# Kernel optimization log

Hardware: AMD Instinct MI355X
Metric: run time of the kernel (lower is better)

## Reference

```python
import jax, jax.numpy as jnp
import numpy as np

N_HEAD = 8
GROUPS = 16
EPS = 1e-5
C = 256


def group_norm(x, gamma, beta):
    # x: (B, C, H, W); GroupNorm over (C//G, H, W) within each group
    B, Cc, H, W = x.shape
    xg = x.reshape(B, GROUPS, Cc // GROUPS, H * W)
    mu = xg.mean(axis=(2, 3), keepdims=True)
    var = xg.var(axis=(2, 3), keepdims=True)
    xn = ((xg - mu) * jax.lax.rsqrt(var + EPS)).reshape(B, Cc, H, W)
    return xn * gamma[None, :, None, None] + beta[None, :, None, None]


def cross_attn(q, k, v, channel):
    # q, k, v: (B, n_head, head_dim, H, W); full bidirectional spatial attention
    B, n, d, H, W = q.shape
    scores = jnp.einsum('bnchw,bncyx->bnhwyx', q, k) / np.float32(np.sqrt(channel))
    attn = jax.nn.softmax(scores.reshape(B, n, H, W, H * W), axis=-1)
    attn = attn.reshape(B, n, H, W, H, W)
    out = jnp.einsum('bnhwyx,bncyx->bnchw', attn, v)
    return out.reshape(B, n * d, H, W)


def conv1x1(w, x, b=None):
    # w: (Cout, Cin), x: (B, Cin, H, W)
    y = jnp.einsum('oc,bchw->bohw', w, x)
    if b is not None:
        y = y + b[None, :, None, None]
    return y


def setup_inputs() -> dict:
    key = jax.random.key(0)
    ks = jax.random.split(key, 8)
    B, H, W = 16, 32, 32
    s = 1.0 / np.sqrt(C)
    return {
        'x_A': jax.random.normal(ks[0], (B, C, H, W), jnp.float32),
        'x_B': jax.random.normal(ks[1], (B, C, H, W), jnp.float32),
        'gA': jnp.ones((C,), jnp.float32),
        'bA': jnp.zeros((C,), jnp.float32),
        'gB': jnp.ones((C,), jnp.float32),
        'bB': jnp.zeros((C,), jnp.float32),
        'WqkvA': jax.random.normal(ks[2], (3 * C, C), jnp.float32) * s,
        'WqkvB': jax.random.normal(ks[3], (3 * C, C), jnp.float32) * s,
        'WoutA': jax.random.normal(ks[4], (C, C), jnp.float32) * s,
        'boutA': jnp.zeros((C,), jnp.float32),
        'WoutB': jax.random.normal(ks[5], (C, C), jnp.float32) * s,
        'boutB': jnp.zeros((C,), jnp.float32),
    }


def reference(x_A, x_B, gA, bA, gB, bB, WqkvA, WqkvB, WoutA, boutA, WoutB, boutB):
    B, Cc, H, W = x_A.shape
    d = Cc // N_HEAD
    norm_A = group_norm(x_A, gA, bA)
    norm_B = group_norm(x_B, gB, bB)
    qkvA = conv1x1(WqkvA, norm_A).reshape(B, N_HEAD, 3 * d, H, W)
    qA, kA, vA = jnp.split(qkvA, 3, axis=2)
    qkvB = conv1x1(WqkvB, norm_B).reshape(B, N_HEAD, 3 * d, H, W)
    qB, kB, vB = jnp.split(qkvB, 3, axis=2)
    # A branch attends query_B -> key/value_A (note scale uses full channel count)
    out_A = conv1x1(WoutA, cross_attn(qB, kA, vA, Cc), boutA) + norm_A
    out_B = conv1x1(WoutB, cross_attn(qA, kB, vB, Cc), boutB) + norm_B
    return (out_A, out_B)
```

## Files before the change

kernel.cpp:

```cpp
#include <hip/hip_runtime.h>
#include <hip/hip_bf16.h>
#include <math.h>

typedef __attribute__((ext_vector_type(8))) short short8;
typedef __attribute__((ext_vector_type(4))) short short4_;
typedef __attribute__((ext_vector_type(4))) float f32x4;
typedef __attribute__((ext_vector_type(4))) unsigned int uint4_;

#define MFMA16(a, b, c) __builtin_amdgcn_mfma_f32_16x16x32_bf16((a), (b), (c), 0, 0, 0)

__device__ __forceinline__ short f2bf(float f) {
  union { float f; unsigned u; } v; v.f = f;
  unsigned r = v.u + 0x7fffu + ((v.u >> 16) & 1u);
  return (short)(r >> 16);
}

__device__ __forceinline__ float bf2f(short s) {
  union { float f; unsigned u; } v; v.u = ((unsigned)(unsigned short)s) << 16;
  return v.f;
}

__device__ __forceinline__ unsigned pktrunc(float a, float b) {
#if __has_builtin(__builtin_amdgcn_perm)
  return __builtin_amdgcn_perm(__builtin_bit_cast(unsigned, b),
                               __builtin_bit_cast(unsigned, a), 0x07060302u);
#else
  return (__builtin_bit_cast(unsigned, b) & 0xffff0000u) |
         (__builtin_bit_cast(unsigned, a) >> 16);
#endif
}

__device__ __forceinline__ float fast_exp2(float x) {
#if __has_builtin(__builtin_amdgcn_exp2f)
  return __builtin_amdgcn_exp2f(x);
#else
  return __exp2f(x);
#endif
}

__device__ __forceinline__ void load_lds16(const void* g, void* l) {
  __builtin_amdgcn_global_load_lds((const __attribute__((address_space(1))) void*)g,
                                   (__attribute__((address_space(3))) void*)l, 16, 0, 0);
}

#define QSCALE 0.09016844005556f

__global__ __launch_bounds__(256) void wcvt_kernel(const float* __restrict__ wqA,
                                                   const float* __restrict__ wqB,
                                                   const float* __restrict__ woA,
                                                   const float* __restrict__ woB,
                                                   short* __restrict__ oqA,
                                                   short* __restrict__ oqB,
                                                   short* __restrict__ ooA,
                                                   short* __restrict__ ooB) {
  int blk = blockIdx.x;
  const float* src; short* dst; int base;
  if (blk < 96) { src = wqA; dst = oqA; base = blk; }
  else if (blk < 192) { src = wqB; dst = oqB; base = blk - 96; }
  else if (blk < 224) { src = woA; dst = ooA; base = blk - 192; }
  else { src = woB; dst = ooB; base = blk - 224; }
  int idx = base * 2048 + threadIdx.x * 8;
  float4 a = *(const float4*)(src + idx);
  float4 b = *(const float4*)(src + idx + 4);
  short8 o;
  o[0] = f2bf(a.x); o[1] = f2bf(a.y); o[2] = f2bf(a.z); o[3] = f2bf(a.w);
  o[4] = f2bf(b.x); o[5] = f2bf(b.y); o[6] = f2bf(b.z); o[7] = f2bf(b.w);
  *(short8*)(dst + idx) = o;
}

__global__ __launch_bounds__(256) void gn_kernel(const float* __restrict__ x,
                                                 const float* __restrict__ gamma,
                                                 const float* __restrict__ beta,
                                                 short* __restrict__ Xt) {
  const int blk = blockIdx.x;
  const int b = blk >> 4, g = blk & 15;
  const int t = threadIdx.x;
  const size_t base = (size_t)blk * 16384;
  const float4* xp = (const float4*)(x + base);
  float s = 0.f, q = 0.f;
  float4 vals[16];
  for (int i = 0; i < 16; ++i) {
    float4 v = xp[t + i * 256];
    vals[i] = v;
    s += v.x + v.y + v.z + v.w;
    q += v.x * v.x + v.y * v.y + v.z * v.z + v.w * v.w;
  }
  __shared__ float rs[256], rq[256];
  rs[t] = s; rq[t] = q;
  __syncthreads();
  for (int o = 128; o > 0; o >>= 1) {
    if (t < o) { rs[t] += rs[t + o]; rq[t] += rq[t + o]; }
    __syncthreads();
  }
  __shared__ float sh_mu, sh_inv;
  if (t == 0) {
    float mu = rs[0] * (1.f / 16384.f);
    float var = rq[0] * (1.f / 16384.f) - mu * mu;
    sh_mu = mu;
    sh_inv = rsqrtf(var + 1e-5f);
  }
  __syncthreads();
  const float mu = sh_mu, inv = sh_inv;
  short tmp[4][16];
#pragma unroll
  for (int i = 0; i < 16; ++i) {
    int c = (g << 4) + i;
    float ga = gamma[c] * inv;
    float be = beta[c] - mu * ga;
    float4 v = vals[i];
    tmp[0][i] = f2bf(v.x * ga + be);
    tmp[1][i] = f2bf(v.y * ga + be);
    tmp[2][i] = f2bf(v.z * ga + be);
    tmp[3][i] = f2bf(v.w * ga + be);
  }
  short* orow = Xt + ((size_t)b * 1024 + 4 * t) * 256 + (g << 4);
#pragma unroll
  for (int j = 0; j < 4; ++j) {
    *(short8*)(orow + j * 256) = *(const short8*)&tmp[j][0];
    *(short8*)(orow + j * 256 + 8) = *(const short8*)&tmp[j][8];
  }
}

__global__ __launch_bounds__(256) void gemm_qkv_kernel(const short* __restrict__ Wb,
                                                       const short* __restrict__ Xt,
                                                       short* __restrict__ Qb,
                                                       short* __restrict__ Kb,
                                                       short* __restrict__ Vb) {
  const int m0 = blockIdx.x * 128, n0 = blockIdx.y * 128, b = blockIdx.z;
  const int t = threadIdx.x;
  __shared__ short As[128 * 64];
  __shared__ short Bs[128 * 64];
  const int w = t >> 6, lane = t & 63, l15 = lane & 15, quad = lane >> 4;
  const int wm = (w >> 1) * 64, wn = (w & 1) * 64;
  const f32x4 z4 = {0.f, 0.f, 0.f, 0.f};
  f32x4 acc[4][4];
  for (int i = 0; i < 4; i++)
    for (int j = 0; j < 4; j++) acc[i][j] = z4;

  const int srow = lane >> 3, cpos = lane & 7;
  const int swz = (cpos ^ srow) * 8;
  const short* wg = Wb + (size_t)(m0 + w * 32 + srow) * 256 + swz;
  const short* xg = Xt + ((size_t)b * 1024 + n0 + w * 32 + srow) * 256 + swz;
  short* lA = &As[(w * 32) * 64];
  short* lB = &Bs[(w * 32) * 64];

  for (int k0 = 0; k0 < 256; k0 += 64) {
    __syncthreads();
#pragma unroll
    for (int qq = 0; qq < 4; ++qq) {
      load_lds16(wg + (size_t)qq * 8 * 256 + k0, lA + qq * 8 * 64);
      load_lds16(xg + (size_t)qq * 8 * 256 + k0, lB + qq * 8 * 64);
    }
    __syncthreads();
#pragma unroll
    for (int s = 0; s < 2; ++s) {
      const int cc = ((s * 4 + quad) ^ (l15 & 7)) * 8;
      short8 af[4], bfb[4];
      for (int i = 0; i < 4; i++) af[i] = *(const short8*)&As[(wm + i * 16 + l15) * 64 + cc];
      for (int j = 0; j < 4; j++) bfb[j] = *(const short8*)&Bs[(wn + j * 16 + l15) * 64 + cc];
      for (int i = 0; i < 4; i++)
        for (int j = 0; j < 4; j++) acc[i][j] = MFMA16(af[i], bfb[j], acc[i][j]);
    }
  }
  for (int i = 0; i < 4; i++) {
    int mi = m0 + wm + i * 16;
    int h = mi / 96;
    int rr = mi - h * 96;
    if (rr < 64) {
      short* dst = (rr < 32) ? Qb : Kb;
      const float mul = (rr < 32) ? QSCALE : 1.0f;
      const int dbase = (rr & 31) + quad * 4;
      const size_t rowb = ((size_t)b * 8 + h) * 1024;
      for (int j = 0; j < 4; j++) {
        int n = n0 + wn + j * 16 + l15;
        short4_ sv;
        for (int r = 0; r < 4; r++) sv[r] = f2bf(acc[i][j][r] * mul);
        *(short4_*)(dst + (rowb + n) * 32 + dbase) = sv;
      }
    } else {
      const int dv = (rr - 64) + quad * 4;
      const size_t vb = (((size_t)b * 8 + h) * 32 + dv) * 1024;
      for (int j = 0; j < 4; j++) {
        int n = n0 + wn + j * 16 + l15;
        for (int r = 0; r < 4; r++) Vb[vb + (size_t)r * 1024 + n] = f2bf(acc[i][j][r]);
      }
    }
  }
}

__global__ __launch_bounds__(256) void attn_kernel(const short* __restrict__ Qb,
                                                   const short* __restrict__ Kb,
                                                   const short* __restrict__ Vb,
                                                   short* __restrict__ AO) {
  const int qt = blockIdx.x, h = blockIdx.y, b = blockIdx.z;
  const int t = threadIdx.x;
  const int w = t >> 6, lane = t & 63, l15 = lane & 15, quad = lane >> 4;
  const size_t hb = (size_t)(b * 8 + h);
  const f32x4 z4 = {0.f, 0.f, 0.f, 0.f};
  __shared__ short Ks[256 * 32];
  __shared__ short Vs[32 * 256];

  const int q0 = qt * 128 + w * 32;
  const short8 bq0 = *(const short8*)(Qb + (hb * 1024 + q0 + l15) * 32 + quad * 8);
  const short8 bq1 = *(const short8*)(Qb + (hb * 1024 + q0 + 16 + l15) * 32 + quad * 8);
  const short* Kg = Kb + hb * 1024 * 32;
  const short* Vg = Vb + hb * 32 * 1024;

  short8 ones;
#pragma unroll
  for (int i = 0; i < 8; ++i) ones[i] = (short)0x3F80;

  const int rk_off = lane >> 2;
  const int ck = lane & 3;
  const int rv_off = lane >> 5;
  const int cv = lane & 31;
  const int kread = l15 * 32 + ((quad ^ ((l15 >> 1) & 3)) * 8);

  f32x4 accO[2][2];
  accO[0][0] = z4; accO[0][1] = z4; accO[1][0] = z4; accO[1][1] = z4;
  f32x4 accL[2];
  accL[0] = z4; accL[1] = z4;

  for (int k0 = 0; k0 < 1024; k0 += 256) {
    __syncthreads();
    for (int p = 0; p < 4; ++p) {
      const int rk = (w * 4 + p) * 16 + rk_off;
      load_lds16(Kg + (size_t)(k0 + rk) * 32 + ((ck ^ ((rk >> 1) & 3)) * 8),
                 &Ks[(w * 4 + p) * 512]);
      const int rv = (w * 4 + p) * 2 + rv_off;
      load_lds16(Vg + (size_t)rv * 1024 + k0 + ((cv ^ (rv & 15)) * 8),
                 &Vs[(w * 4 + p) * 512]);
    }
    __syncthreads();

    for (int pr = 0; pr < 8; ++pr) {
      const short8 ak0 = *(const short8*)&Ks[(2 * pr) * 512 + kread];
      const short8 ak1 = *(const short8*)&Ks[(2 * pr + 1) * 512 + kread];
      f32x4 st00 = MFMA16(ak0, bq0, z4);
      f32x4 st10 = MFMA16(ak1, bq0, z4);
      f32x4 st01 = MFMA16(ak0, bq1, z4);
      f32x4 st11 = MFMA16(ak1, bq1, z4);
      union { short8 s; uint4_ u; } apv0, apv1;
      {
        float p0 = fast_exp2(st00[0]), p1 = fast_exp2(st00[1]);
        float p2 = fast_exp2(st00[2]), p3 = fast_exp2(st00[3]);
        float p4 = fast_exp2(st10[0]), p5 = fast_exp2(st10[1]);
        float p6 = fast_exp2(st10[2]), p7 = fast_exp2(st10[3]);
        apv0.u[0] = pktrunc(p0, p1); apv0.u[1] = pktrunc(p2, p3);
        apv0.u[2] = pktrunc(p4, p5); apv0.u[3] = pktrunc(p6, p7);
      }
      {
        float p0 = fast_exp2(st01[0]), p1 = fast_exp2(st01[1]);
        float p2 = fast_exp2(st01[2]), p3 = fast_exp2(st01[3]);
        float p4 = fast_exp2(st11[0]), p5 = fast_exp2(st11[1]);
        float p6 = fast_exp2(st11[2]), p7 = fast_exp2(st11[3]);
        apv1.u[0] = pktrunc(p0, p1); apv1.u[1] = pktrunc(p2, p3);
        apv1.u[2] = pktrunc(p4, p5); apv1.u[3] = pktrunc(p6, p7);
      }
      const int cg = pr * 4 + (quad >> 1);
      const int so = (quad & 1) * 4;
      for (int dvt = 0; dvt < 2; ++dvt) {
        const int dvrow = (dvt * 16 + l15) * 256;
        union { short8 s; short4_ hh[2]; } bv;
        bv.hh[0] = *(const short4_*)&Vs[dvrow + ((cg ^ l15) * 8) + so];
        bv.hh[1] = *(const short4_*)&Vs[dvrow + (((cg + 2) ^ l15) * 8) + so];
        accO[0][dvt] = MFMA16(apv0.s, bv.s, accO[0][dvt]);
        accO[1][dvt] = MFMA16(apv1.s, bv.s, accO[1][dvt]);
      }
      accL[0] = MFMA16(apv0.s, ones, accL[0]);
      accL[1] = MFMA16(apv1.s, ones, accL[1]);
    }
  }

  for (int s = 0; s < 2; ++s) {
    for (int r = 0; r < 4; r++) {
      float inv = 1.0f / accL[s][r];
      int sq = q0 + s * 16 + quad * 4 + r;
      short* orow = AO + ((size_t)b * 1024 + sq) * 256 + h * 32 + l15;
      orow[0] = f2bf(accO[s][0][r] * inv);
      orow[16] = f2bf(accO[s][1][r] * inv);
    }
  }
}

__global__ __launch_bounds__(256) void gemm_out_kernel(const short* __restrict__ Wob,
                                                       const short* __restrict__ ao,
                                                       const float* __restrict__ bias,
                                                       const short* __restrict__ Xt,
                                                       float* __restrict__ out) {
  const int m0 = blockIdx.x * 128, n0 = blockIdx.y * 128, b = blockIdx.z;
  const int t = threadIdx.x;
  __shared__ short smem[128 * 64 * 2];
  short* As = smem;
  short* Bs = smem + 128 * 64;
  const int w = t >> 6, lane = t & 63, l15 = lane & 15, quad = lane >> 4;
  const int wm = (w >> 1) * 64, wn = (w & 1) * 64;
  const f32x4 z4 = {0.f, 0.f, 0.f, 0.f};
  f32x4 acc[4][4];
  for (int i = 0; i < 4; i++)
    for (int j = 0; j < 4; j++) acc[i][j] = z4;

  const int srow = lane >> 3, cpos = lane & 7;
  const int swz = (cpos ^ srow) * 8;
  const short* wg = Wob + (size_t)(m0 + w * 32 + srow) * 256 + swz;
  const short* xg = ao + ((size_t)b * 1024 + n0 + w * 32 + srow) * 256 + swz;
  short* lA = &As[(w * 32) * 64];
  short* lB = &Bs[(w * 32) * 64];

  for (int k0 = 0; k0 < 256; k0 += 64) {
    __syncthreads();
#pragma unroll
    for (int qq = 0; qq < 4; ++qq) {
      load_lds16(wg + (size_t)qq * 8 * 256 + k0, lA + qq * 8 * 64);
      load_lds16(xg + (size_t)qq * 8 * 256 + k0, lB + qq * 8 * 64);
    }
    __syncthreads();
#pragma unroll
    for (int s = 0; s < 2; ++s) {
      const int cc = ((s * 4 + quad) ^ (l15 & 7)) * 8;
      short8 af[4], bfb[4];
      for (int i = 0; i < 4; i++) af[i] = *(const short8*)&As[(wm + i * 16 + l15) * 64 + cc];
      for (int j = 0; j < 4; j++) bfb[j] = *(const short8*)&Bs[(wn + j * 16 + l15) * 64 + cc];
      for (int i = 0; i < 4; i++)
        for (int j = 0; j < 4; j++) acc[i][j] = MFMA16(af[i], bfb[j], acc[i][j]);
    }
  }

  __syncthreads();
  {
    const int rrow = lane >> 4, rc = lane & 15;
    for (int qq = 0; qq < 8; ++qq) {
      int row = w * 32 + qq * 4 + rrow;
      load_lds16(Xt + ((size_t)b * 1024 + n0 + row) * 256 + m0 + ((rc ^ (row & 15)) * 8),
                 &smem[(w * 32 + qq * 4) * 128]);
    }
  }
  __syncthreads();

  for (int i = 0; i < 4; i++)
    for (int j = 0; j < 4; j++) {
      int m = m0 + wm + i * 16 + quad * 4;
      int nl = wn + j * 16 + l15;
      int n = n0 + nl;
      size_t off = ((size_t)b * 256 + m) * 1024 + n;
      const int chunk = (wm >> 3) + i * 2 + (quad >> 1);
      short4_ rv = *(const short4_*)&smem[nl * 128 + ((chunk ^ (nl & 15)) * 8) + (quad & 1) * 4];
      for (int r = 0; r < 4; r++)
        out[off + (size_t)r * 1024] = acc[i][j][r] + bias[m + r] + bf2f(rv[r]);
    }
}

extern "C" void kernel_launch(void* const* d_in, const int* in_sizes, int n_in,
                              void* d_out, int out_size, void* d_ws, size_t ws_size,
                              hipStream_t stream) {
  const float* xA = (const float*)d_in[0];
  const float* xB = (const float*)d_in[1];
  const float* gA = (const float*)d_in[2];
  const float* bA = (const float*)d_in[3];
  const float* gB = (const float*)d_in[4];
  const float* bB = (const float*)d_in[5];
  const float* WqkvA = (const float*)d_in[6];
  const float* WqkvB = (const float*)d_in[7];
  const float* WoutA = (const float*)d_in[8];
  const float* boutA = (const float*)d_in[9];
  const float* WoutB = (const float*)d_in[10];
  const float* boutB = (const float*)d_in[11];
  float* out = (float*)d_out;
  char* ws = (char*)d_ws;
  short* XtA = (short*)(ws);
  short* XtB = (short*)(ws + 8388608);
  short* QbA = (short*)(ws + 16777216);
  short* KbA = (short*)(ws + 25165824);
  short* VbA = (short*)(ws + 33554432);
  short* QbB = (short*)(ws + 41943040);
  short* KbB = (short*)(ws + 50331648);
  short* VbB = (short*)(ws + 58720256);
  short* aoA = (short*)(ws + 67108864);
  short* aoB = (short*)(ws + 75497472);
  short* WqbA = (short*)(ws + 83886080);
  short* WqbB = (short*)(ws + 84279296);
  short* WobA = (short*)(ws + 84672512);
  short* WobB = (short*)(ws + 84803584);

  wcvt_kernel<<<256, 256, 0, stream>>>(WqkvA, WqkvB, WoutA, WoutB, WqbA, WqbB, WobA, WobB);
  gn_kernel<<<256, 256, 0, stream>>>(xA, gA, bA, XtA);
  gn_kernel<<<256, 256, 0, stream>>>(xB, gB, bB, XtB);
  gemm_qkv_kernel<<<dim3(6, 8, 16), 256, 0, stream>>>(WqbA, XtA, QbA, KbA, VbA);
  gemm_qkv_kernel<<<dim3(6, 8, 16), 256, 0, stream>>>(WqbB, XtB, QbB, KbB, VbB);
  attn_kernel<<<dim3(8, 8, 16), 256, 0, stream>>>(QbB, KbA, VbA, aoA);
  attn_kernel<<<dim3(8, 8, 16), 256, 0, stream>>>(QbA, KbB, VbB, aoB);
  gemm_out_kernel<<<dim3(2, 8, 16), 256, 0, stream>>>(WobA, aoA, boutA, XtA, out);
  gemm_out_kernel<<<dim3(2, 8, 16), 256, 0, stream>>>(WobB, aoB, boutB, XtB, out + 4194304);
}
```

Measured before the change: 226.6 us.

## Merge A/B branch launches into single kernels and fuse weight conversion with GroupNorm

Collapses the nine launches into four. Weight conversion and both GroupNorms now share one prep kernel, and each GEMM and attention kernel processes both branches through the grid z dimension, with workspace offsets fixed by macros. The grid order is also changed (n-tile first for the QKV GEMM, batch first for attention), which may alter L2 reuse of K/V and weights. Packed bf16 conversions replace scalar f2bf calls. The aim is to cut launch gaps and tail effects and fill the GPU better, at the cost of more index arithmetic and the hardcoded layout.

```diff
diff --git a/kernel.cpp b/kernel.cpp
--- a/kernel.cpp
+++ b/kernel.cpp
@@ -9,6 +9,21 @@
 
 #define MFMA16(a, b, c) __builtin_amdgcn_mfma_f32_16x16x32_bf16((a), (b), (c), 0, 0, 0)
 
+#define OFF_XTA   0
+#define OFF_XTB   8388608
+#define OFF_QBA   16777216
+#define OFF_KBA   25165824
+#define OFF_VBA   33554432
+#define OFF_QBB   41943040
+#define OFF_KBB   50331648
+#define OFF_VBB   58720256
+#define OFF_AOA   67108864
+#define OFF_AOB   75497472
+#define OFF_WQA   83886080
+#define OFF_WQB   84279296
+#define OFF_WOA   84672512
+#define OFF_WOB   84803584
+
 __device__ __forceinline__ short f2bf(float f) {
   union { float f; unsigned u; } v; v.f = f;
   unsigned r = v.u + 0x7fffu + ((v.u >> 16) & 1u);
@@ -18,6 +33,12 @@
 __device__ __forceinline__ float bf2f(short s) {
   union { float f; unsigned u; } v; v.u = ((unsigned)(unsigned short)s) << 16;
   return v.f;
+}
+
+__device__ __forceinline__ unsigned pk2bf(float a, float b) {
+  union { __hip_bfloat162 h2; unsigned u; } cv;
+  cv.h2 = __float22bfloat162_rn(float2{a, b});
+  return cv.u;
 }
 
 __device__ __forceinline__ unsigned pktrunc(float a, float b) {
@@ -45,37 +66,42 @@
 
 #define QSCALE 0.09016844005556f
 
-__global__ __launch_bounds__(256) void wcvt_kernel(const float* __restrict__ wqA,
+__global__ __launch_bounds__(256) void prep_kernel(const float* __restrict__ xA,
+                                                   const float* __restrict__ xB,
+                                                   const float* __restrict__ gA,
+                                                   const float* __restrict__ bA,
+                                                   const float* __restrict__ gB,
+                                                   const float* __restrict__ bB,
+                                                   const float* __restrict__ wqA,
                                                    const float* __restrict__ wqB,
                                                    const float* __restrict__ woA,
                                                    const float* __restrict__ woB,
-                                                   short* __restrict__ oqA,
-                                                   short* __restrict__ oqB,
-                                                   short* __restrict__ ooA,
-                                                   short* __restrict__ ooB) {
-  int blk = blockIdx.x;
-  const float* src; short* dst; int base;
-  if (blk < 96) { src = wqA; dst = oqA; base = blk; }
-  else if (blk < 192) { src = wqB; dst = oqB; base = blk - 96; }
-  else if (blk < 224) { src = woA; dst = ooA; base = blk - 192; }
-  else { src = woB; dst = ooB; base = blk - 224; }
-  int idx = base * 2048 + threadIdx.x * 8;
-  float4 a = *(const float4*)(src + idx);
-  float4 b = *(const float4*)(src + idx + 4);
-  short8 o;
-  o[0] = f2bf(a.x); o[1] = f2bf(a.y); o[2] = f2bf(a.z); o[3] = f2bf(a.w);
-  o[4] = f2bf(b.x); o[5] = f2bf(b.y); o[6] = f2bf(b.z); o[7] = f2bf(b.w);
-  *(short8*)(dst + idx) = o;
-}
-
-__global__ __launch_bounds__(256) void gn_kernel(const float* __restrict__ x,
-                                                 const float* __restrict__ gamma,
-                                                 const float* __restrict__ beta,
-                                                 short* __restrict__ Xt) {
+                                                   char* __restrict__ ws) {
   const int blk = blockIdx.x;
-  const int b = blk >> 4, g = blk & 15;
   const int t = threadIdx.x;
-  const size_t base = (size_t)blk * 16384;
+  if (blk >= 512) {
+    int wb = blk - 512;
+    const float* src; short* dst; int base;
+    if (wb < 96) { src = wqA; dst = (short*)(ws + OFF_WQA); base = wb; }
+    else if (wb < 192) { src = wqB; dst = (short*)(ws + OFF_WQB); base = wb - 96; }
+    else if (wb < 224) { src = woA; dst = (short*)(ws + OFF_WOA); base = wb - 192; }
+    else { src = woB; dst = (short*)(ws + OFF_WOB); base = wb - 224; }
+    int idx = base * 2048 + t * 8;
+    float4 a = *(const float4*)(src + idx);
+    float4 b = *(const float4*)(src + idx + 4);
+    uint4_ o;
+    o[0] = pk2bf(a.x, a.y); o[1] = pk2bf(a.z, a.w);
+    o[2] = pk2bf(b.x, b.y); o[3] = pk2bf(b.z, b.w);
+    *(uint4_*)(dst + idx) = o;
+    return;
+  }
+  const int br = blk >> 8, sub = blk & 255;
+  const int b = sub >> 4, g = sub & 15;
+  const float* x = br ? xB : xA;
+  const float* gamma = br ? gB : gA;
+  const float* beta = br ? bB : bA;
+  short* Xt = (short*)(ws + (br ? OFF_XTB : OFF_XTA));
+  const size_t base = (size_t)sub * 16384;
   const float4* xp = (const float4*)(x + base);
   float s = 0.f, q = 0.f;
   float4 vals[16];
@@ -101,32 +127,34 @@
   }
   __syncthreads();
   const float mu = sh_mu, inv = sh_inv;
-  short tmp[4][16];
-#pragma unroll
-  for (int i = 0; i < 16; ++i) {
+  unsigned td[4][8];
+#pragma unroll
+  for (int i = 0; i < 16; i += 2) {
     int c = (g << 4) + i;
-    float ga = gamma[c] * inv;
-    float be = beta[c] - mu * ga;
-    float4 v = vals[i];
-    tmp[0][i] = f2bf(v.x * ga + be);
-    tmp[1][i] = f2bf(v.y * ga + be);
-    tmp[2][i] = f2bf(v.z * ga + be);
-    tmp[3][i] = f2bf(v.w * ga + be);
+    float ga0 = gamma[c] * inv, be0 = beta[c] - mu * ga0;
+    float ga1 = gamma[c + 1] * inv, be1 = beta[c + 1] - mu * ga1;
+    float4 v0 = vals[i], v1 = vals[i + 1];
+    td[0][i >> 1] = pk2bf(v0.x * ga0 + be0, v1.x * ga1 + be1);
+    td[1][i >> 1] = pk2bf(v0.y * ga0 + be0, v1.y * ga1 + be1);
+    td[2][i >> 1] = pk2bf(v0.z * ga0 + be0, v1.z * ga1 + be1);
+    td[3][i >> 1] = pk2bf(v0.w * ga0 + be0, v1.w * ga1 + be1);
   }
   short* orow = Xt + ((size_t)b * 1024 + 4 * t) * 256 + (g << 4);
 #pragma unroll
   for (int j = 0; j < 4; ++j) {
-    *(short8*)(orow + j * 256) = *(const short8*)&tmp[j][0];
-    *(short8*)(orow + j * 256 + 8) = *(const short8*)&tmp[j][8];
-  }
-}
-
-__global__ __launch_bounds__(256) void gemm_qkv_kernel(const short* __restrict__ Wb,
-                                                       const short* __restrict__ Xt,
-                                                       short* __restrict__ Qb,
-                                                       short* __restrict__ Kb,
-                                                       short* __restrict__ Vb) {
-  const int m0 = blockIdx.x * 128, n0 = blockIdx.y * 128, b = blockIdx.z;
+    *(uint4_*)(orow + j * 256) = *(const uint4_*)&td[j][0];
+    *(uint4_*)(orow + j * 256 + 8) = *(const uint4_*)&td[j][4];
+  }
+}
+
+__global__ __launch_bounds__(256) void gemm_qkv_kernel(char* __restrict__ ws) {
+  const int n0 = blockIdx.x * 128, m0 = blockIdx.y * 128;
+  const int b = blockIdx.z & 15, br = blockIdx.z >> 4;
+  const short* Wb = (const short*)(ws + (br ? OFF_WQB : OFF_WQA));
+  const short* Xt = (const short*)(ws + (br ? OFF_XTB : OFF_XTA));
+  short* Qb = (short*)(ws + (br ? OFF_QBB : OFF_QBA));
+  short* Kb = Qb + 4194304;
+  short* Vb = Qb + 8388608;
   const int t = threadIdx.x;
   __shared__ short As[128 * 64];
   __shared__ short Bs[128 * 64];
@@ -173,9 +201,10 @@
       const size_t rowb = ((size_t)b * 8 + h) * 1024;
       for (int j = 0; j < 4; j++) {
         int n = n0 + wn + j * 16 + l15;
-        short4_ sv;
-        for (int r = 0; r < 4; r++) sv[r] = f2bf(acc[i][j][r] * mul);
-        *(short4_*)(dst + (rowb + n) * 32 + dbase) = sv;
+        union { unsigned u[2]; short4_ s; } uv;
+        uv.u[0] = pk2bf(acc[i][j][0] * mul, acc[i][j][1] * mul);
+        uv.u[1] = pk2bf(acc[i][j][2] * mul, acc[i][j][3] * mul);
+        *(short4_*)(dst + (rowb + n) * 32 + dbase) = uv.s;
       }
     } else {
       const int dv = (rr - 64) + quad * 4;
@@ -188,11 +217,13 @@
   }
 }
 
-__global__ __launch_bounds__(256) void attn_kernel(const short* __restrict__ Qb,
-                                                   const short* __restrict__ Kb,
-                                                   const short* __restrict__ Vb,
-                                                   short* __restrict__ AO) {
-  const int qt = blockIdx.x, h = blockIdx.y, b = blockIdx.z;
+__global__ __launch_bounds__(256) void attn_kernel(char* __restrict__ ws) {
+  const int b = blockIdx.x, h = blockIdx.y;
+  const int qt = blockIdx.z & 7, br = blockIdx.z >> 3;
+  const short* Qb = (const short*)(ws + (br ? OFF_QBA : OFF_QBB));
+  const short* Kb = (const short*)(ws + (br ? OFF_KBB : OFF_KBA));
+  const short* Vb = Kb + 4194304;
+  short* AO = (short*)(ws + (br ? OFF_AOB : OFF_AOA));
   const int t = threadIdx.x;
   const int w = t >> 6, lane = t & 63, l15 = lane & 15, quad = lane >> 4;
   const size_t hb = (size_t)(b * 8 + h);
@@ -283,12 +314,17 @@
   }
 }
 
-__global__ __launch_bounds__(256) void gemm_out_kernel(const short* __restrict__ Wob,
-                                                       const short* __restrict__ ao,
-                                                       const float* __restrict__ bias,
-                                                       const short* __restrict__ Xt,
-                                                       float* __restrict__ out) {
-  const int m0 = blockIdx.x * 128, n0 = blockIdx.y * 128, b = blockIdx.z;
+__global__ __launch_bounds__(256) void gemm_out_kernel(char* __restrict__ ws,
+                                                       const float* __restrict__ boutA,
+                                                       const float* __restrict__ boutB,
+                                                       float* __restrict__ outbase) {
+  const int m0 = blockIdx.x * 128, n0 = blockIdx.y * 128;
+  const int b = blockIdx.z & 15, br = blockIdx.z >> 4;
+  const short* Wob = (const short*)(ws + (br ? OFF_WOB : OFF_WOA));
+  const short* ao = (const short*)(ws + (br ? OFF_AOB : OFF_AOA));
+  const float* bias = br ? boutB : boutA;
+  const short* Xt = (const short*)(ws + (br ? OFF_XTB : OFF_XTA));
+  float* out = outbase + (br ? 4194304 : 0);
   const int t = threadIdx.x;
   __shared__ short smem[128 * 64 * 2];
   short* As = smem;
@@ -367,28 +403,10 @@
   const float* boutB = (const float*)d_in[11];
   float* out = (float*)d_out;
   char* ws = (char*)d_ws;
-  short* XtA = (short*)(ws);
-  short* XtB = (short*)(ws + 8388608);
-  short* QbA = (short*)(ws + 16777216);
-  short* KbA = (short*)(ws + 25165824);
-  short* VbA = (short*)(ws + 33554432);
-  short* QbB = (short*)(ws + 41943040);
-  short* KbB = (short*)(ws + 50331648);
-  short* VbB = (short*)(ws + 58720256);
-  short* aoA = (short*)(ws + 67108864);
-  short* aoB = (short*)(ws + 75497472);
-  short* WqbA = (short*)(ws + 83886080);
-  short* WqbB = (short*)(ws + 84279296);
-  short* WobA = (short*)(ws + 84672512);
-  short* WobB = (short*)(ws + 84803584);
-
-  wcvt_kernel<<<256, 256, 0, stream>>>(WqkvA, WqkvB, WoutA, WoutB, WqbA, WqbB, WobA, WobB);
-  gn_kernel<<<256, 256, 0, stream>>>(xA, gA, bA, XtA);
-  gn_kernel<<<256, 256, 0, stream>>>(xB, gB, bB, XtB);
-  gemm_qkv_kernel<<<dim3(6, 8, 16), 256, 0, stream>>>(WqbA, XtA, QbA, KbA, VbA);
-  gemm_qkv_kernel<<<dim3(6, 8, 16), 256, 0, stream>>>(WqbB, XtB, QbB, KbB, VbB);
-  attn_kernel<<<dim3(8, 8, 16), 256, 0, stream>>>(QbB, KbA, VbA, aoA);
-  attn_kernel<<<dim3(8, 8, 16), 256, 0, stream>>>(QbA, KbB, VbB, aoB);
-  gemm_out_kernel<<<dim3(2, 8, 16), 256, 0, stream>>>(WobA, aoA, boutA, XtA, out);
-  gemm_out_kernel<<<dim3(2, 8, 16), 256, 0, stream>>>(WobB, aoB, boutB, XtB, out + 4194304);
-}
+
+  prep_kernel<<<768, 256, 0, stream>>>(xA, xB, gA, bA, gB, bB,
+                                       WqkvA, WqkvB, WoutA, WoutB, ws);
+  gemm_qkv_kernel<<<dim3(8, 6, 32), 256, 0, stream>>>(ws);
+  attn_kernel<<<dim3(16, 8, 16), 256, 0, stream>>>(ws);
+  gemm_out_kernel<<<dim3(2, 8, 32), 256, 0, stream>>>(ws, boutA, boutB, out);
+}
```

After: 195.1 us. 13.9% less time.
